# Kernel tuning notes

Hardware: AMD Instinct MI355X
Metric: run time of the kernel (lower is better)

Reference implementation:

```python
import jax, jax.numpy as jnp
import numpy as np

N, K, C, OUT = 2048, 14, 512, 512
SCALE = 4.0
BN_EPS = 1e-5


def _edge_lists(k):
    # pairs i<j with i,j != k-1 and adj[i,j] > 0 (adj is fully connected ones)
    ei, ej = [], []
    for i in range(k - 1):
        for j in range(i + 1, k - 1):
            ei.append(i)
            ej.append(j)
    return np.asarray(ei, np.int32), np.asarray(ej, np.int32)


def setup_inputs() -> dict:
    key = jax.random.key(0)
    k0, k1, k2, k3 = jax.random.split(key, 4)
    ei, ej = _edge_lists(K)
    std = 0.02
    return {
        "inputs": jax.random.normal(k0, (N, K, C), dtype=jnp.float32),
        "adj": jnp.ones((K, K), dtype=jnp.float32),
        "edge_i": jnp.asarray(ei),
        "edge_j": jnp.asarray(ej),
        "gamma": jnp.ones((C,), dtype=jnp.float32),
        "beta": jnp.zeros((C,), dtype=jnp.float32),
        "w_direct": jax.random.normal(k1, (C,), dtype=jnp.float32) * std,
        "W_merged": jax.random.normal(k2, (OUT, C), dtype=jnp.float32) * std,
        "W_orig": jax.random.normal(k3, (OUT, C), dtype=jnp.float32) * std,
    }


def reference(inputs, adj, edge_i, edge_j, gamma, beta, w_direct, W_merged, W_orig):
    n, k, c = inputs.shape
    # --- learn_adj ---
    global_feat = inputs[:, k - 1 : k, :]                      # [N,1,c]
    distances = jnp.abs(inputs - global_feat)                  # [N,k,c]
    # pairwise gaps only on the static edge list (i<j, non-global, adj>0)
    gap = 15.0 * (distances[:, edge_i, :] - distances[:, edge_j, :])  # [N,E,c]
    # BatchNorm1d over channel c, batch stats over (N, E), biased variance
    mean = jnp.mean(gap, axis=(0, 1))
    var = jnp.mean(jnp.square(gap - mean), axis=(0, 1))
    bn = (gap - mean) * (gamma / jnp.sqrt(var + BN_EPS)) + beta        # [N,E,c]
    a = jax.nn.sigmoid(SCALE * jnp.einsum("nec,c->ne", bn, w_direct))  # [N,E]
    adj2 = jnp.ones((n, k, k), dtype=inputs.dtype)
    adj2 = adj2.at[:, edge_i, edge_j].set(2.0 * a)
    adj2 = adj2.at[:, edge_j, edge_i].set(2.0 * (1.0 - a))
    new_adj = adj2 * adj[None, :, :]
    norm = jnp.sum(jnp.abs(new_adj), axis=2, keepdims=True)    # L1 row norm
    new_adj = new_adj / jnp.maximum(norm, 1e-12)
    # --- graph conv ---
    agg = jnp.einsum("nij,njc->nic", new_adj, inputs)          # [N,k,c]
    merged = jax.nn.relu(jnp.einsum("nkc,oc->nko", agg, W_merged))
    original = jnp.einsum("nkc,oc->nko", inputs, W_orig)
    return merged + original
```

## Files before the change

### kernel.cpp

```cpp
#include <hip/hip_runtime.h>
#include <stdint.h>

#define K_NODES 14
#define C_DIM   512
#define OUT_DIM 512
#define N_EDGE  78

typedef float  f32x4  __attribute__((ext_vector_type(4)));
typedef __bf16 bf16x8 __attribute__((ext_vector_type(8)));

__device__ __forceinline__ unsigned short f2bf(float f) {
    unsigned int u = __builtin_bit_cast(unsigned int, f);
    unsigned int r = (u + 0x7fffu + ((u >> 16) & 1u)) >> 16;
    return (unsigned short)r;
}
__device__ __forceinline__ float bf2f(unsigned short s) {
    return __builtin_bit_cast(float, (unsigned int)s << 16);
}

__device__ __forceinline__ void async16(const void* g, void* l) {
    __builtin_amdgcn_global_load_lds(
        (const __attribute__((address_space(1))) unsigned int*)g,
        (__attribute__((address_space(3))) unsigned int*)l, 16, 0, 0);
}

__global__ __launch_bounds__(1024) void stats_partial(
    const float* __restrict__ x, float* __restrict__ part,
    unsigned short* __restrict__ xbf,
    const float* __restrict__ Wm, const float* __restrict__ Wo,
    unsigned short* __restrict__ wmbf, unsigned short* __restrict__ wobf)
{
    int t  = threadIdx.x;
    int q  = t & 127;
    int sn = t >> 7;
    int n  = blockIdx.x * 8 + sn;
    size_t base = (size_t)n * K_NODES * C_DIM + q * 4;

    f32x4 g = *(const f32x4*)(x + base + 13 * C_DIM);
    ushort4 gb; gb.x=f2bf(g.x); gb.y=f2bf(g.y); gb.z=f2bf(g.z); gb.w=f2bf(g.w);
    *(ushort4*)(xbf + base + 13 * C_DIM) = gb;

    float S10=0,S11=0,S12=0,S13=0, S20=0,S21=0,S22=0,S23=0, Sw0=0,Sw1=0,Sw2=0,Sw3=0;
    #pragma unroll
    for (int k = 0; k < 13; ++k) {
        f32x4 v = *(const f32x4*)(x + base + k * C_DIM);
        ushort4 vb; vb.x=f2bf(v.x); vb.y=f2bf(v.y); vb.z=f2bf(v.z); vb.w=f2bf(v.w);
        *(ushort4*)(xbf + base + k * C_DIM) = vb;
        float wk = (float)(12 - 2 * k);
        float d0=fabsf(v.x-g.x), d1=fabsf(v.y-g.y), d2=fabsf(v.z-g.z), d3=fabsf(v.w-g.w);
        S10+=d0; S11+=d1; S12+=d2; S13+=d3;
        S20+=d0*d0; S21+=d1*d1; S22+=d2*d2; S23+=d3*d3;
        Sw0+=wk*d0; Sw1+=wk*d1; Sw2+=wk*d2; Sw3+=wk*d3;
    }
    f32x4 as = (f32x4){15.f*Sw0, 15.f*Sw1, 15.f*Sw2, 15.f*Sw3};
    f32x4 aq = (f32x4){225.f*(13.f*S20 - S10*S10), 225.f*(13.f*S21 - S11*S11),
                       225.f*(13.f*S22 - S12*S12), 225.f*(13.f*S23 - S13*S13)};

    __shared__ f32x4 redS[8][128];
    __shared__ f32x4 redQ[8][128];
    redS[sn][q] = as;
    redQ[sn][q] = aq;
    __syncthreads();
    if (sn == 0) {
        f32x4 s = redS[0][q], z = redQ[0][q];
        #pragma unroll
        for (int r = 1; r < 8; ++r) { s += redS[r][q]; z += redQ[r][q]; }
        *(f32x4*)(part + (size_t)blockIdx.x * 1024 + q * 4)       = s;
        *(f32x4*)(part + (size_t)blockIdx.x * 1024 + 512 + q * 4) = z;
    }
    int i0 = blockIdx.x * 1024 + t;
    wmbf[i0] = f2bf(Wm[i0]);
    wobf[i0] = f2bf(Wo[i0]);
}

__global__ __launch_bounds__(1024) void finalize_stats(
    const float* __restrict__ part, float inv_ne,
    const float* __restrict__ gamma, const float* __restrict__ beta,
    const float* __restrict__ wdir, float* __restrict__ u, float* __restrict__ bconst)
{
    int c = threadIdx.x & 511;
    int h = threadIdx.x >> 9;
    float s = 0.f, q = 0.f;
    for (int b = h * 128; b < h * 128 + 128; b += 16) {
        #pragma unroll
        for (int t = 0; t < 16; ++t) {
            s += part[(size_t)(b + t) * 1024 + c];
            q += part[(size_t)(b + t) * 1024 + 512 + c];
        }
    }
    __shared__ float sh_s[512], sh_q[512], red[512];
    if (h == 0) { sh_s[c] = s; sh_q[c] = q; }
    __syncthreads();
    if (h == 1) { sh_s[c] += s; sh_q[c] += q; }
    __syncthreads();
    if (h == 0) {
        float mean = sh_s[c] * inv_ne;
        float var  = sh_q[c] * inv_ne - mean * mean;
        float sc   = gamma[c] / sqrtf(var + 1e-5f);
        u[c] = sc * wdir[c];
        red[c] = (beta[c] - mean * sc) * wdir[c];
    }
    __syncthreads();
    for (int st = 256; st > 0; st >>= 1) {
        if (threadIdx.x < st) red[threadIdx.x] += red[threadIdx.x + st];
        __syncthreads();
    }
    if (threadIdx.x == 0) *bconst = red[0];
}

__global__ __launch_bounds__(256) void fuse_graph(
    const unsigned short* __restrict__ xbf, const float* __restrict__ adj,
    const int* __restrict__ ei, const int* __restrict__ ej,
    const float* __restrict__ u, const float* __restrict__ bconst,
    unsigned short* __restrict__ aggbf)
{
    __shared__ float WL[2][196];
    __shared__ float Dp[2][2][13];
    __shared__ float invL[2][14];
    int wv = threadIdx.x >> 6, lane = threadIdx.x & 63;
    int sp = wv >> 1;
    int h  = wv & 1;
    int n  = blockIdx.x * 2 + sp;
    size_t base = (size_t)n * K_NODES * C_DIM + h * 256 + lane * 4;

    float xf[K_NODES][4];
    #pragma unroll
    for (int k = 0; k < K_NODES; ++k) {
        uint2 raw = *(const uint2*)(xbf + base + k * C_DIM);
        xf[k][0]=bf2f(raw.x&0xffff); xf[k][1]=bf2f(raw.x>>16);
        xf[k][2]=bf2f(raw.y&0xffff); xf[k][3]=bf2f(raw.y>>16);
    }
    f32x4 uv = *(const f32x4*)(u + h * 256 + lane * 4);

    #pragma unroll
    for (int k = 0; k < 13; ++k) {
        float p = fabsf(xf[k][0]-xf[13][0])*uv.x + fabsf(xf[k][1]-xf[13][1])*uv.y
                + fabsf(xf[k][2]-xf[13][2])*uv.z + fabsf(xf[k][3]-xf[13][3])*uv.w;
        #pragma unroll
        for (int off = 1; off < 64; off <<= 1) p += __shfl_xor(p, off, 64);
        if (lane == 0) Dp[sp][h][k] = p;
    }
    __syncthreads();

    if (h == 0) {
        for (int e = lane; e < N_EDGE; e += 64) {
            int ii = ei[e], jj = ej[e];
            float Di = Dp[sp][0][ii] + Dp[sp][1][ii];
            float Dj = Dp[sp][0][jj] + Dp[sp][1][jj];
            float z = 4.0f * (15.f * (Di - Dj) + *bconst);
            float a = 1.f / (1.f + expf(-z));
            WL[sp][ii * K_NODES + jj] = adj[ii * K_NODES + jj] * (2.f * a);
            WL[sp][jj * K_NODES + ii] = adj[jj * K_NODES + ii] * (2.f * (1.f - a));
        }
    } else {
        for (int idx = lane; idx < K_NODES * K_NODES; idx += 64) {
            int i = idx / K_NODES, j = idx - i * K_NODES;
            if (i == j || i == 13 || j == 13) WL[sp][idx] = adj[idx];
        }
    }
    __syncthreads();
    if (h == 0 && lane < K_NODES) {
        float s = 0.f;
        #pragma unroll
        for (int j = 0; j < K_NODES; ++j) s += fabsf(WL[sp][lane * K_NODES + j]);
        invL[sp][lane] = 1.f / fmaxf(s, 1e-12f);
    }
    __syncthreads();

    #pragma unroll
    for (int i = 0; i < K_NODES; ++i) {
        float s0=0.f,s1=0.f,s2=0.f,s3=0.f;
        #pragma unroll
        for (int j = 0; j < K_NODES; ++j) {
            float w = WL[sp][i * K_NODES + j];
            s0 += w*xf[j][0]; s1 += w*xf[j][1]; s2 += w*xf[j][2]; s3 += w*xf[j][3];
        }
        float wi = invL[sp][i];
        uint2 r;
        r.x = (unsigned int)f2bf(s0*wi) | ((unsigned int)f2bf(s1*wi) << 16);
        r.y = (unsigned int)f2bf(s2*wi) | ((unsigned int)f2bf(s3*wi) << 16);
        *(uint2*)(aggbf + base + i * C_DIM) = r;
    }
}

#define TM 128
#define TN 128
#define BK 64

__global__ __launch_bounds__(256) void gemm_fused(
    const unsigned short* __restrict__ Aagg, const unsigned short* __restrict__ Axin,
    const unsigned short* __restrict__ Bwm,  const unsigned short* __restrict__ Bwo,
    float* __restrict__ out)
{
    __shared__ unsigned short lA[TM * BK];
    __shared__ unsigned short lB[TN * BK];
    int tid  = threadIdx.x;
    int lane = tid & 63;
    int wave = tid >> 6;
    int wr = wave >> 1, wc = wave & 1;
    int bm = blockIdx.x * TM;
    int bn = blockIdx.y * TN;

    f32x4 acc[4][4];
    #pragma unroll
    for (int i = 0; i < 4; ++i)
        #pragma unroll
        for (int j = 0; j < 4; ++j) acc[i][j] = (f32x4){0.f, 0.f, 0.f, 0.f};

    int lrow = lane & 15;
    int xorv = lane & 7;
    int srow  = tid >> 3;
    int lcu   = ((tid & 7) ^ (srow & 7)) * 8;

    #pragma unroll
    for (int pass = 0; pass < 2; ++pass) {
        const unsigned short* A = pass ? Axin : Aagg;
        const unsigned short* B = pass ? Bwo  : Bwm;
        for (int kb = 0; kb < C_DIM; kb += BK) {
            __syncthreads();
            #pragma unroll
            for (int it = 0; it < 4; ++it) {
                int row = it * 32 + srow;
                async16(A + (size_t)(bm + row) * C_DIM + kb + lcu,
                        &lA[(size_t)(it * 256 + wave * 64) * 8]);
                async16(B + (size_t)(bn + row) * C_DIM + kb + lcu,
                        &lB[(size_t)(it * 256 + wave * 64) * 8]);
            }
            __syncthreads();
            #pragma unroll
            for (int ks = 0; ks < 2; ++ks) {
                int pchunk = ((ks * 4 + (lane >> 4)) ^ xorv) * 8;
                bf16x8 af[4], bfr[4];
                #pragma unroll
                for (int i = 0; i < 4; ++i)
                    af[i] = *(const bf16x8*)&lA[(wr * 64 + i * 16 + lrow) * BK + pchunk];
                #pragma unroll
                for (int j = 0; j < 4; ++j)
                    bfr[j] = *(const bf16x8*)&lB[(wc * 64 + j * 16 + lrow) * BK + pchunk];
                #pragma unroll
                for (int i = 0; i < 4; ++i)
                    #pragma unroll
                    for (int j = 0; j < 4; ++j)
                        acc[i][j] = __builtin_amdgcn_mfma_f32_16x16x32_bf16(
                            af[i], bfr[j], acc[i][j], 0, 0, 0);
            }
        }
        if (pass == 0) {
            #pragma unroll
            for (int i = 0; i < 4; ++i)
                #pragma unroll
                for (int j = 0; j < 4; ++j)
                    #pragma unroll
                    for (int r = 0; r < 4; ++r)
                        acc[i][j][r] = fmaxf(acc[i][j][r], 0.f);
        }
    }

    int orow0 = bm + wr * 64 + (lane >> 4) * 4;
    int ocol0 = bn + wc * 64 + (lane & 15);
    #pragma unroll
    for (int i = 0; i < 4; ++i)
        #pragma unroll
        for (int j = 0; j < 4; ++j)
            #pragma unroll
            for (int r = 0; r < 4; ++r)
                out[(size_t)(orow0 + i * 16 + r) * OUT_DIM + (ocol0 + j * 16)] = acc[i][j][r];
}

extern "C" void kernel_launch(void* const* d_in, const int* in_sizes, int n_in,
                              void* d_out, int out_size, void* d_ws, size_t ws_size,
                              hipStream_t stream)
{
    const float* x     = (const float*)d_in[0];
    const float* adj   = (const float*)d_in[1];
    const int*   ei    = (const int*)d_in[2];
    const int*   ej    = (const int*)d_in[3];
    const float* gamma = (const float*)d_in[4];
    const float* beta  = (const float*)d_in[5];
    const float* wdir  = (const float*)d_in[6];
    const float* Wm    = (const float*)d_in[7];
    const float* Wo    = (const float*)d_in[8];
    float* out = (float*)d_out;

    int N = in_sizes[0] / (K_NODES * C_DIM);
    int M = N * K_NODES;

    float* ws_f   = (float*)d_ws;
    float* u      = ws_f + 1024;
    float* bconst = ws_f + 1536;
    float* part   = ws_f + 2048;
    char*  wsb    = (char*)d_ws;
    size_t off    = (size_t)(2048 + 256 * 1024) * sizeof(float);
    unsigned short* wmbf  = (unsigned short*)(wsb + off);  off += (size_t)OUT_DIM * C_DIM * 2;
    unsigned short* wobf  = (unsigned short*)(wsb + off);  off += (size_t)OUT_DIM * C_DIM * 2;
    unsigned short* xbf   = (unsigned short*)(wsb + off);  off += (size_t)M * C_DIM * 2;
    unsigned short* aggbf = (unsigned short*)(wsb + off);

    float inv_ne = 1.0f / ((float)N * (float)N_EDGE);

    hipLaunchKernelGGL(stats_partial, dim3(N / 8), dim3(1024), 0, stream,
                       x, part, xbf, Wm, Wo, wmbf, wobf);
    hipLaunchKernelGGL(finalize_stats, dim3(1), dim3(1024), 0, stream,
                       part, inv_ne, gamma, beta, wdir, u, bconst);
    hipLaunchKernelGGL(fuse_graph, dim3(N / 2), dim3(256), 0, stream,
                       xbf, adj, ei, ej, u, bconst, aggbf);
    hipLaunchKernelGGL(gemm_fused, dim3(M / TM, OUT_DIM / TN), dim3(256), 0, stream,
                       aggbf, xbf, wmbf, wobf, out);
}
```

Measured before the change: 193.7 us.

## Double-buffer GEMM LDS tiles and parallelize BN stats finalize across blocks

The fused GEMM now keeps two LDS buffers and issues the async loads for the next K-slice (crossing from the merged pass into the original pass) while MFMAs run on the current slice. This hides global-to-LDS latency and removes one barrier per iteration, at the cost of twice the LDS per block, which may lower occupancy. The stats finalize kernel is split from a single 1024-thread block into 8 blocks of 64 channels each, using a wave shuffle reduction. Each block writes a partial bias that fuse_graph sums, so the serial single-block tail gets shorter.

```diff
diff --git a/kernel.cpp b/kernel.cpp
--- a/kernel.cpp
+++ b/kernel.cpp
@@ -73,45 +73,41 @@
     wobf[i0] = f2bf(Wo[i0]);
 }
 
-__global__ __launch_bounds__(1024) void finalize_stats(
+__global__ __launch_bounds__(256) void finalize_stats(
     const float* __restrict__ part, float inv_ne,
     const float* __restrict__ gamma, const float* __restrict__ beta,
-    const float* __restrict__ wdir, float* __restrict__ u, float* __restrict__ bconst)
-{
-    int c = threadIdx.x & 511;
-    int h = threadIdx.x >> 9;
+    const float* __restrict__ wdir, float* __restrict__ u, float* __restrict__ bpart)
+{
+    int lane = threadIdx.x & 63;
+    int wv   = threadIdx.x >> 6;
+    int c    = blockIdx.x * 64 + lane;
     float s = 0.f, q = 0.f;
-    for (int b = h * 128; b < h * 128 + 128; b += 16) {
-        #pragma unroll
-        for (int t = 0; t < 16; ++t) {
-            s += part[(size_t)(b + t) * 1024 + c];
-            q += part[(size_t)(b + t) * 1024 + 512 + c];
-        }
-    }
-    __shared__ float sh_s[512], sh_q[512], red[512];
-    if (h == 0) { sh_s[c] = s; sh_q[c] = q; }
-    __syncthreads();
-    if (h == 1) { sh_s[c] += s; sh_q[c] += q; }
-    __syncthreads();
-    if (h == 0) {
-        float mean = sh_s[c] * inv_ne;
-        float var  = sh_q[c] * inv_ne - mean * mean;
+    #pragma unroll 8
+    for (int r = wv; r < 256; r += 4) {
+        s += part[(size_t)r * 1024 + c];
+        q += part[(size_t)r * 1024 + 512 + c];
+    }
+    __shared__ float shs[4][64], shq[4][64];
+    shs[wv][lane] = s; shq[wv][lane] = q;
+    __syncthreads();
+    if (wv == 0) {
+        s = shs[0][lane] + shs[1][lane] + shs[2][lane] + shs[3][lane];
+        q = shq[0][lane] + shq[1][lane] + shq[2][lane] + shq[3][lane];
+        float mean = s * inv_ne;
+        float var  = q * inv_ne - mean * mean;
         float sc   = gamma[c] / sqrtf(var + 1e-5f);
         u[c] = sc * wdir[c];
-        red[c] = (beta[c] - mean * sc) * wdir[c];
-    }
-    __syncthreads();
-    for (int st = 256; st > 0; st >>= 1) {
-        if (threadIdx.x < st) red[threadIdx.x] += red[threadIdx.x + st];
-        __syncthreads();
-    }
-    if (threadIdx.x == 0) *bconst = red[0];
+        float b = (beta[c] - mean * sc) * wdir[c];
+        #pragma unroll
+        for (int off = 1; off < 64; off <<= 1) b += __shfl_xor(b, off, 64);
+        if (lane == 0) bpart[blockIdx.x] = b;
+    }
 }
 
 __global__ __launch_bounds__(256) void fuse_graph(
     const unsigned short* __restrict__ xbf, const float* __restrict__ adj,
     const int* __restrict__ ei, const int* __restrict__ ej,
-    const float* __restrict__ u, const float* __restrict__ bconst,
+    const float* __restrict__ u, const float* __restrict__ bpart,
     unsigned short* __restrict__ aggbf)
 {
     __shared__ float WL[2][196];
@@ -143,11 +139,14 @@
     __syncthreads();
 
     if (h == 0) {
+        float bc = 0.f;
+        #pragma unroll
+        for (int b8 = 0; b8 < 8; ++b8) bc += bpart[b8];
         for (int e = lane; e < N_EDGE; e += 64) {
             int ii = ei[e], jj = ej[e];
             float Di = Dp[sp][0][ii] + Dp[sp][1][ii];
             float Dj = Dp[sp][0][jj] + Dp[sp][1][jj];
-            float z = 4.0f * (15.f * (Di - Dj) + *bconst);
+            float z = 4.0f * (15.f * (Di - Dj) + bc);
             float a = 1.f / (1.f + expf(-z));
             WL[sp][ii * K_NODES + jj] = adj[ii * K_NODES + jj] * (2.f * a);
             WL[sp][jj * K_NODES + ii] = adj[jj * K_NODES + ii] * (2.f * (1.f - a));
@@ -192,8 +191,8 @@
     const unsigned short* __restrict__ Bwm,  const unsigned short* __restrict__ Bwo,
     float* __restrict__ out)
 {
-    __shared__ unsigned short lA[TM * BK];
-    __shared__ unsigned short lB[TN * BK];
+    __shared__ unsigned short lA[2][TM * BK];
+    __shared__ unsigned short lB[2][TN * BK];
     int tid  = threadIdx.x;
     int lane = tid & 63;
     int wave = tid >> 6;
@@ -212,40 +211,45 @@
     int srow  = tid >> 3;
     int lcu   = ((tid & 7) ^ (srow & 7)) * 8;
 
-    #pragma unroll
-    for (int pass = 0; pass < 2; ++pass) {
-        const unsigned short* A = pass ? Axin : Aagg;
-        const unsigned short* B = pass ? Bwo  : Bwm;
-        for (int kb = 0; kb < C_DIM; kb += BK) {
-            __syncthreads();
-            #pragma unroll
-            for (int it = 0; it < 4; ++it) {
-                int row = it * 32 + srow;
-                async16(A + (size_t)(bm + row) * C_DIM + kb + lcu,
-                        &lA[(size_t)(it * 256 + wave * 64) * 8]);
-                async16(B + (size_t)(bn + row) * C_DIM + kb + lcu,
-                        &lB[(size_t)(it * 256 + wave * 64) * 8]);
-            }
-            __syncthreads();
-            #pragma unroll
-            for (int ks = 0; ks < 2; ++ks) {
-                int pchunk = ((ks * 4 + (lane >> 4)) ^ xorv) * 8;
-                bf16x8 af[4], bfr[4];
-                #pragma unroll
-                for (int i = 0; i < 4; ++i)
-                    af[i] = *(const bf16x8*)&lA[(wr * 64 + i * 16 + lrow) * BK + pchunk];
+#define STAGE(buf, Ap, Bp, kb)                                              \
+    _Pragma("unroll")                                                        \
+    for (int it = 0; it < 4; ++it) {                                         \
+        int row = it * 32 + srow;                                            \
+        async16((Ap) + (size_t)(bm + row) * C_DIM + (kb) + lcu,              \
+                &lA[buf][(it * 256 + wave * 64) * 8]);                       \
+        async16((Bp) + (size_t)(bn + row) * C_DIM + (kb) + lcu,              \
+                &lB[buf][(it * 256 + wave * 64) * 8]);                       \
+    }
+
+    STAGE(0, Aagg, Bwm, 0);
+    __syncthreads();
+
+    #pragma unroll
+    for (int ph = 0; ph < 16; ++ph) {
+        const int cur = ph & 1;
+        if (ph < 15) {
+            const unsigned short* Ap = ((ph + 1) < 8) ? Aagg : Axin;
+            const unsigned short* Bp = ((ph + 1) < 8) ? Bwm  : Bwo;
+            STAGE(cur ^ 1, Ap, Bp, ((ph + 1) & 7) * BK);
+        }
+        #pragma unroll
+        for (int ks = 0; ks < 2; ++ks) {
+            int pchunk = ((ks * 4 + (lane >> 4)) ^ xorv) * 8;
+            bf16x8 af[4], bfr[4];
+            #pragma unroll
+            for (int i = 0; i < 4; ++i)
+                af[i] = *(const bf16x8*)&lA[cur][(wr * 64 + i * 16 + lrow) * BK + pchunk];
+            #pragma unroll
+            for (int j = 0; j < 4; ++j)
+                bfr[j] = *(const bf16x8*)&lB[cur][(wc * 64 + j * 16 + lrow) * BK + pchunk];
+            #pragma unroll
+            for (int i = 0; i < 4; ++i)
                 #pragma unroll
                 for (int j = 0; j < 4; ++j)
-                    bfr[j] = *(const bf16x8*)&lB[(wc * 64 + j * 16 + lrow) * BK + pchunk];
-                #pragma unroll
-                for (int i = 0; i < 4; ++i)
-                    #pragma unroll
-                    for (int j = 0; j < 4; ++j)
-                        acc[i][j] = __builtin_amdgcn_mfma_f32_16x16x32_bf16(
-                            af[i], bfr[j], acc[i][j], 0, 0, 0);
-            }
-        }
-        if (pass == 0) {
+                    acc[i][j] = __builtin_amdgcn_mfma_f32_16x16x32_bf16(
+                        af[i], bfr[j], acc[i][j], 0, 0, 0);
+        }
+        if (ph == 7) {
             #pragma unroll
             for (int i = 0; i < 4; ++i)
                 #pragma unroll
@@ -254,7 +258,9 @@
                     for (int r = 0; r < 4; ++r)
                         acc[i][j][r] = fmaxf(acc[i][j][r], 0.f);
         }
-    }
+        __syncthreads();
+    }
+#undef STAGE
 
     int orow0 = bm + wr * 64 + (lane >> 4) * 4;
     int ocol0 = bn + wc * 64 + (lane & 15);
@@ -287,7 +293,7 @@
 
     float* ws_f   = (float*)d_ws;
     float* u      = ws_f + 1024;
-    float* bconst = ws_f + 1536;
+    float* bpart  = ws_f + 1536;
     float* part   = ws_f + 2048;
     char*  wsb    = (char*)d_ws;
     size_t off    = (size_t)(2048 + 256 * 1024) * sizeof(float);
@@ -300,10 +306,10 @@
 
     hipLaunchKernelGGL(stats_partial, dim3(N / 8), dim3(1024), 0, stream,
                        x, part, xbf, Wm, Wo, wmbf, wobf);
-    hipLaunchKernelGGL(finalize_stats, dim3(1), dim3(1024), 0, stream,
-                       part, inv_ne, gamma, beta, wdir, u, bconst);
+    hipLaunchKernelGGL(finalize_stats, dim3(8), dim3(256), 0, stream,
+                       part, inv_ne, gamma, beta, wdir, u, bpart);
     hipLaunchKernelGGL(fuse_graph, dim3(N / 2), dim3(256), 0, stream,
-                       xbf, adj, ei, ej, u, bconst, aggbf);
+                       xbf, adj, ei, ej, u, bpart, aggbf);
     hipLaunchKernelGGL(gemm_fused, dim3(M / TM, OUT_DIM / TN), dim3(256), 0, stream,
                        aggbf, xbf, wmbf, wobf, out);
 }
```

After: 183.3 us. 1.06x faster.
